# Optimization experiments

Hardware: AMD Instinct MI355X
Metric: run time of the kernel (lower is better)

Reference implementation:

```python
import jax, jax.numpy as jnp
import numpy as np

B, S, D, H = 4, 2048, 768, 12
HD = D // H  # head dim = 64


def setup_inputs() -> dict:
    key = jax.random.key(0)
    ks = jax.random.split(key, 8)
    w_scale = 0.02
    return {
        "x": jax.random.normal(ks[0], (B, S, D), dtype=jnp.float32),
        "Wq": jax.random.normal(ks[1], (D, D), dtype=jnp.float32) * w_scale,
        "bq": jnp.zeros((D,), dtype=jnp.float32),
        "Wk": jax.random.normal(ks[2], (D, D), dtype=jnp.float32) * w_scale,
        "Wv": jax.random.normal(ks[3], (D, D), dtype=jnp.float32) * w_scale,
        "bv": jnp.zeros((D,), dtype=jnp.float32),
        "Wo": jax.random.normal(ks[4], (D, D), dtype=jnp.float32) * w_scale,
        "bo": jnp.zeros((D,), dtype=jnp.float32),
    }


def reference(x, Wq, bq, Wk, Wv, bv, Wo, bo):
    # Self-attention branch (xa=None, no kv_cache), causal mask enabled.
    q = x @ Wq + bq                       # [B,S,D]; key proj has no bias
    k = x @ Wk
    v = x @ Wv + bv

    def split_heads(t):
        return t.reshape(B, S, H, HD).transpose(0, 2, 1, 3)  # [B,H,S,HD]

    q, k, v = split_heads(q), split_heads(k), split_heads(v)

    scale = float(HD) ** -0.5  # applied once to qk == (hd**-0.25 on q and k)
    qk = jnp.einsum("bhqd,bhkd->bhqk", q, k) * scale  # [B,H,S,S]

    # dynamic causal mask: -inf where kv index > q index
    causal = jnp.where(
        jnp.arange(S)[:, None] < jnp.arange(S)[None, :], -jnp.inf, 0.0
    ).astype(jnp.float32)
    qk = qk + causal

    w = jax.nn.softmax(qk.astype(jnp.float32), axis=-1).astype(q.dtype)
    out = jnp.einsum("bhqk,bhkd->bhqd", w, v)          # [B,H,S,HD]
    out = out.transpose(0, 2, 1, 3).reshape(B, S, D)    # [B,S,D]
    output = out @ Wo + bo
    return output, jax.lax.stop_gradient(qk)
```

## Files before the change

### kernel.cpp

```cpp
#include <hip/hip_runtime.h>
#include <cmath>

#define BB 4
#define SS 2048
#define DD 768
#define HH 12
#define HDD 64
#define MROWS (BB * SS)
#define NHEADS (BB * HH)

#define MASK_SENTINEL (-3.0e38f)

typedef float f32x4v __attribute__((ext_vector_type(4)));

__device__ __forceinline__ void nt_store4(float* p, float a, float b, float c,
                                          float d) {
    f32x4v t = {a, b, c, d};
    __builtin_nontemporal_store(t, reinterpret_cast<f32x4v*>(p));
}

template <bool SPLIT_HEADS>
__global__ __launch_bounds__(128) void gemm768(const float* __restrict__ A,
                                               const float* __restrict__ W,
                                               const float* __restrict__ bias,
                                               float* __restrict__ out) {
    __shared__ float As[16][132];
    __shared__ float Bs[16][68];

    const int tid = threadIdx.x;
    const int tx = tid & 7;
    const int ty = tid >> 3;
    const int m0 = blockIdx.y * 128;
    const int n0 = blockIdx.x * 64;

    const int br = tid >> 3;
    const int bc = (tid & 7) * 8;

    float acc[8][8] = {};

    for (int k0 = 0; k0 < 768; k0 += 16) {
        float4 av[4];
        const float* ap = &A[(size_t)(m0 + tid) * 768 + k0];
#pragma unroll
        for (int c = 0; c < 4; ++c) av[c] = reinterpret_cast<const float4*>(ap)[c];
        float4 bv[2];
        const float* bp = &W[(size_t)(k0 + br) * 768 + n0 + bc];
        bv[0] = reinterpret_cast<const float4*>(bp)[0];
        bv[1] = reinterpret_cast<const float4*>(bp)[1];

        if (k0 != 0) __syncthreads();
#pragma unroll
        for (int c = 0; c < 4; ++c) {
            As[c * 4 + 0][tid] = av[c].x;
            As[c * 4 + 1][tid] = av[c].y;
            As[c * 4 + 2][tid] = av[c].z;
            As[c * 4 + 3][tid] = av[c].w;
        }
        *reinterpret_cast<float4*>(&Bs[br][bc]) = bv[0];
        *reinterpret_cast<float4*>(&Bs[br][bc + 4]) = bv[1];
        __syncthreads();

#pragma unroll
        for (int kk = 0; kk < 16; ++kk) {
            const float4 a0 = *reinterpret_cast<const float4*>(&As[kk][ty * 8]);
            const float4 a1 = *reinterpret_cast<const float4*>(&As[kk][ty * 8 + 4]);
            const float4 b0 = *reinterpret_cast<const float4*>(&Bs[kk][tx * 8]);
            const float4 b1 = *reinterpret_cast<const float4*>(&Bs[kk][tx * 8 + 4]);
            const float af[8] = {a0.x, a0.y, a0.z, a0.w, a1.x, a1.y, a1.z, a1.w};
            const float bf[8] = {b0.x, b0.y, b0.z, b0.w, b1.x, b1.y, b1.z, b1.w};
#pragma unroll
            for (int i = 0; i < 8; ++i)
#pragma unroll
                for (int j = 0; j < 8; ++j)
                    acc[i][j] = fmaf(af[i], bf[j], acc[i][j]);
        }
    }

    float bn[8];
#pragma unroll
    for (int j = 0; j < 8; ++j) bn[j] = (bias != nullptr) ? bias[n0 + tx * 8 + j] : 0.f;

    const int h = n0 >> 6;
#pragma unroll
    for (int i = 0; i < 8; ++i) {
        const int m = m0 + ty * 8 + i;
        float r[8];
#pragma unroll
        for (int j = 0; j < 8; ++j) r[j] = acc[i][j] + bn[j];
        if (SPLIT_HEADS) {
            const int b = m >> 11;
            const int s = m & 2047;
            float* op = &out[(((size_t)(b * HH + h)) * SS + s) * HDD + tx * 8];
            *reinterpret_cast<float4*>(op) = make_float4(r[0], r[1], r[2], r[3]);
            *reinterpret_cast<float4*>(op + 4) = make_float4(r[4], r[5], r[6], r[7]);
        } else {
            float* op = &out[(size_t)m * 768 + n0 + tx * 8];
            *reinterpret_cast<float4*>(op) = make_float4(r[0], r[1], r[2], r[3]);
            *reinterpret_cast<float4*>(op + 4) = make_float4(r[4], r[5], r[6], r[7]);
        }
    }
}

__global__ __launch_bounds__(256) void attn_flash(const float* __restrict__ q,
                                                  const float* __restrict__ k,
                                                  const float* __restrict__ v,
                                                  float* __restrict__ qk_out,
                                                  float* __restrict__ attn_out) {
    __shared__ float Ks[64][68];
    __shared__ float Vs[64][68];

    const int tid = threadIdx.x;
    const int oct = tid & 7;
    const int rg = (tid >> 3) & 31;
    const int d0 = oct * 8;
    const int pair = blockIdx.x;
    const int bh = blockIdx.y;
    const size_t head_base = (size_t)bh * SS * HDD;
    const float scale = 0.125f;
    const int b_idx = bh / HH;
    const int h_idx = bh % HH;

    const int sr = tid >> 2;
    const int scb = (tid & 3) * 16;

    const int rsel = oct >> 2;
    const int g = oct & 3;

#pragma unroll 1
    for (int leg = 0; leg < 2; ++leg) {
        const int tq = (leg == 0) ? (31 - pair) : pair;
        const int q0 = tq * 64;
        const int qr0 = q0 + rg;
        const int qr1 = q0 + rg + 32;

        float4 q0reg[2], q1reg[2];
        {
            const float* qp0 = q + head_base + (size_t)qr0 * HDD + d0;
            const float* qp1 = q + head_base + (size_t)qr1 * HDD + d0;
            q0reg[0] = reinterpret_cast<const float4*>(qp0)[0];
            q0reg[1] = reinterpret_cast<const float4*>(qp0)[1];
            q1reg[0] = reinterpret_cast<const float4*>(qp1)[0];
            q1reg[1] = reinterpret_cast<const float4*>(qp1)[1];
        }

        float4 o0[2], o1[2];
#pragma unroll
        for (int c = 0; c < 2; ++c) {
            o0[c] = make_float4(0.f, 0.f, 0.f, 0.f);
            o1[c] = make_float4(0.f, 0.f, 0.f, 0.f);
        }
        float m0i = -INFINITY, l0 = 0.f;
        float m1i = -INFINITY, l1 = 0.f;

        float* qk_row0 = qk_out + ((size_t)bh * SS + qr0) * SS;
        float* qk_row1 = qk_out + ((size_t)bh * SS + qr1) * SS;

        const int kt_end = tq + 1;

        for (int kt = 0; kt < kt_end; ++kt) {
            float4 kreg[4], vreg[4];
            {
                const float* kp = k + head_base + (size_t)(kt * 64 + sr) * HDD + scb;
                const float* vp = v + head_base + (size_t)(kt * 64 + sr) * HDD + scb;
#pragma unroll
                for (int i = 0; i < 4; ++i) {
                    kreg[i] = reinterpret_cast<const float4*>(kp)[i];
                    vreg[i] = reinterpret_cast<const float4*>(vp)[i];
                }
            }
            __syncthreads();
#pragma unroll
            for (int i = 0; i < 4; ++i) {
                *reinterpret_cast<float4*>(&Ks[sr][scb + i * 4]) = kreg[i];
                *reinterpret_cast<float4*>(&Vs[sr][scb + i * 4]) = vreg[i];
            }
            __syncthreads();

            for (int jc = 0; jc < 64; jc += 16) {
                float s0[16], s1[16];
#pragma unroll
                for (int jj = 0; jj < 16; ++jj) {
                    const int j = jc + jj;
                    const float4 kv0 = *reinterpret_cast<const float4*>(&Ks[j][d0]);
                    const float4 kv1 =
                        *reinterpret_cast<const float4*>(&Ks[j][d0 + 4]);
                    float a0 = 0.f, a1 = 0.f;
                    a0 = fmaf(q0reg[0].x, kv0.x, a0);
                    a0 = fmaf(q0reg[0].y, kv0.y, a0);
                    a0 = fmaf(q0reg[0].z, kv0.z, a0);
                    a0 = fmaf(q0reg[0].w, kv0.w, a0);
                    a0 = fmaf(q0reg[1].x, kv1.x, a0);
                    a0 = fmaf(q0reg[1].y, kv1.y, a0);
                    a0 = fmaf(q0reg[1].z, kv1.z, a0);
                    a0 = fmaf(q0reg[1].w, kv1.w, a0);
                    a1 = fmaf(q1reg[0].x, kv0.x, a1);
                    a1 = fmaf(q1reg[0].y, kv0.y, a1);
                    a1 = fmaf(q1reg[0].z, kv0.z, a1);
                    a1 = fmaf(q1reg[0].w, kv0.w, a1);
                    a1 = fmaf(q1reg[1].x, kv1.x, a1);
                    a1 = fmaf(q1reg[1].y, kv1.y, a1);
                    a1 = fmaf(q1reg[1].z, kv1.z, a1);
                    a1 = fmaf(q1reg[1].w, kv1.w, a1);
                    a0 += __shfl_xor(a0, 1);
                    a0 += __shfl_xor(a0, 2);
                    a0 += __shfl_xor(a0, 4);
                    a1 += __shfl_xor(a1, 1);
                    a1 += __shfl_xor(a1, 2);
                    a1 += __shfl_xor(a1, 4);
                    const int jg = kt * 64 + j;
                    s0[jj] = (jg > qr0) ? -INFINITY : a0 * scale;
                    s1[jj] = (jg > qr1) ? -INFINITY : a1 * scale;
                }

                {
                    float w[4];
#pragma unroll
                    for (int t = 0; t < 4; ++t) {
                        const float x01 = (g & 1) ? s0[4 + t] : s0[t];
                        const float x23 = (g & 1) ? s0[12 + t] : s0[8 + t];
                        const float xs = (g & 2) ? x23 : x01;
                        const float y01 = (g & 1) ? s1[4 + t] : s1[t];
                        const float y23 = (g & 1) ? s1[12 + t] : s1[8 + t];
                        const float ys = (g & 2) ? y23 : y01;
                        w[t] = fmaxf(rsel ? ys : xs, MASK_SENTINEL);
                    }
                    float* dst = (rsel ? qk_row1 : qk_row0) + kt * 64 + jc + g * 4;
                    nt_store4(dst, w[0], w[1], w[2], w[3]);
                }

                float mc0 = s0[0], mc1 = s1[0];
#pragma unroll
                for (int jj = 1; jj < 16; ++jj) {
                    mc0 = fmaxf(mc0, s0[jj]);
                    mc1 = fmaxf(mc1, s1[jj]);
                }
                const float mn0 = fmaxf(m0i, mc0);
                const float mn1 = fmaxf(m1i, mc1);
                const bool dead0 = (mn0 == -INFINITY);
                const bool dead1 = (mn1 == -INFINITY);
                const float alpha0 = dead0 ? 1.f : __expf(m0i - mn0);
                const float alpha1 = dead1 ? 1.f : __expf(m1i - mn1);
                const float sub0 = dead0 ? 0.f : mn0;
                const float sub1 = dead1 ? 0.f : mn1;
                m0i = mn0;
                m1i = mn1;
                float ps0 = 0.f, ps1 = 0.f;
#pragma unroll
                for (int jj = 0; jj < 16; ++jj) {
                    s0[jj] = __expf(s0[jj] - sub0);
                    s1[jj] = __expf(s1[jj] - sub1);
                    ps0 += s0[jj];
                    ps1 += s1[jj];
                }
                l0 = l0 * alpha0 + ps0;
                l1 = l1 * alpha1 + ps1;
#pragma unroll
                for (int c = 0; c < 2; ++c) {
                    o0[c].x *= alpha0; o0[c].y *= alpha0;
                    o0[c].z *= alpha0; o0[c].w *= alpha0;
                    o1[c].x *= alpha1; o1[c].y *= alpha1;
                    o1[c].z *= alpha1; o1[c].w *= alpha1;
                }
#pragma unroll
                for (int jj = 0; jj < 16; ++jj) {
                    const float4 vv0 =
                        *reinterpret_cast<const float4*>(&Vs[jc + jj][d0]);
                    const float4 vv1 =
                        *reinterpret_cast<const float4*>(&Vs[jc + jj][d0 + 4]);
                    const float p0 = s0[jj];
                    const float p1 = s1[jj];
                    o0[0].x = fmaf(p0, vv0.x, o0[0].x);
                    o0[0].y = fmaf(p0, vv0.y, o0[0].y);
                    o0[0].z = fmaf(p0, vv0.z, o0[0].z);
                    o0[0].w = fmaf(p0, vv0.w, o0[0].w);
                    o0[1].x = fmaf(p0, vv1.x, o0[1].x);
                    o0[1].y = fmaf(p0, vv1.y, o0[1].y);
                    o0[1].z = fmaf(p0, vv1.z, o0[1].z);
                    o0[1].w = fmaf(p0, vv1.w, o0[1].w);
                    o1[0].x = fmaf(p1, vv0.x, o1[0].x);
                    o1[0].y = fmaf(p1, vv0.y, o1[0].y);
                    o1[0].z = fmaf(p1, vv0.z, o1[0].z);
                    o1[0].w = fmaf(p1, vv0.w, o1[0].w);
                    o1[1].x = fmaf(p1, vv1.x, o1[1].x);
                    o1[1].y = fmaf(p1, vv1.y, o1[1].y);
                    o1[1].z = fmaf(p1, vv1.z, o1[1].z);
                    o1[1].w = fmaf(p1, vv1.w, o1[1].w);
                }
            }
        }

        for (int base = kt_end * 64; base < SS; base += 32) {
            nt_store4(&qk_row0[base + oct * 4], MASK_SENTINEL, MASK_SENTINEL,
                      MASK_SENTINEL, MASK_SENTINEL);
            nt_store4(&qk_row1[base + oct * 4], MASK_SENTINEL, MASK_SENTINEL,
                      MASK_SENTINEL, MASK_SENTINEL);
        }

        const float inv0 = 1.0f / l0;
        const float inv1 = 1.0f / l1;
        float* op0 = attn_out + ((size_t)(b_idx * SS + qr0)) * DD + h_idx * HDD + d0;
        float* op1 = attn_out + ((size_t)(b_idx * SS + qr1)) * DD + h_idx * HDD + d0;
#pragma unroll
        for (int c = 0; c < 2; ++c) {
            float4 t0 = o0[c], t1 = o1[c];
            t0.x *= inv0; t0.y *= inv0; t0.z *= inv0; t0.w *= inv0;
            t1.x *= inv1; t1.y *= inv1; t1.z *= inv1; t1.w *= inv1;
            reinterpret_cast<float4*>(op0)[c] = t0;
            reinterpret_cast<float4*>(op1)[c] = t1;
        }
    }
}

extern "C" void kernel_launch(void* const* d_in, const int* in_sizes, int n_in,
                              void* d_out, int out_size, void* d_ws, size_t ws_size,
                              hipStream_t stream) {
    const float* x = (const float*)d_in[0];
    const float* Wq = (const float*)d_in[1];
    const float* bq = (const float*)d_in[2];
    const float* Wk = (const float*)d_in[3];
    const float* Wv = (const float*)d_in[4];
    const float* bv = (const float*)d_in[5];
    const float* Wo = (const float*)d_in[6];
    const float* bo = (const float*)d_in[7];

    float* out = (float*)d_out;
    float* qk = out + (size_t)BB * SS * DD;

    const size_t seg = (size_t)BB * SS * DD;
    float* qws = (float*)d_ws;
    float* kws = qws + seg;
    float* vws = qws + 2 * seg;
    float* aws = qws + 3 * seg;

    const dim3 gblk(128);
    const dim3 ggrid(DD / 64, MROWS / 128);

    gemm768<true><<<ggrid, gblk, 0, stream>>>(x, Wq, bq, qws);
    gemm768<true><<<ggrid, gblk, 0, stream>>>(x, Wk, nullptr, kws);
    gemm768<true><<<ggrid, gblk, 0, stream>>>(x, Wv, bv, vws);

    attn_flash<<<dim3(16, NHEADS), dim3(256), 0, stream>>>(qws, kws, vws, qk, aws);

    gemm768<false><<<ggrid, gblk, 0, stream>>>(aws, Wo, bo, out);
}
```

Before: 2.772 ms.

## Convert projections to fp16 MFMA GEMMs with pre-converted transposed weights

Replaces the fp32 SIMT projection GEMMs with an fp16 MFMA 16x16x32 kernel. Activations and weights are first converted to fp16, with the weights also transposed, in separate kernels. The attention kernel now writes its output in fp16 so the output projection can consume it directly. It also drops the nontemporal stores on the qk matrix in favour of plain float4 stores. Precision drops to fp16 inputs, and the GEMM epilogue now uses scalar, less coalesced stores.

```diff
diff --git a/kernel.cpp b/kernel.cpp
--- a/kernel.cpp
+++ b/kernel.cpp
@@ -11,92 +11,141 @@
 
 #define MASK_SENTINEL (-3.0e38f)
 
-typedef float f32x4v __attribute__((ext_vector_type(4)));
-
-__device__ __forceinline__ void nt_store4(float* p, float a, float b, float c,
-                                          float d) {
-    f32x4v t = {a, b, c, d};
-    __builtin_nontemporal_store(t, reinterpret_cast<f32x4v*>(p));
+typedef _Float16 f16;
+typedef _Float16 f16x8 __attribute__((ext_vector_type(8)));
+typedef float f32x4 __attribute__((ext_vector_type(4)));
+
+__global__ __launch_bounds__(256) void cvt_f32_f16(const float* __restrict__ in,
+                                                   f16* __restrict__ out, int n8) {
+    const int i = blockIdx.x * 256 + threadIdx.x;
+    if (i >= n8) return;
+    const float4 v0 = reinterpret_cast<const float4*>(in)[i * 2];
+    const float4 v1 = reinterpret_cast<const float4*>(in)[i * 2 + 1];
+    const f16x8 r = {(f16)v0.x, (f16)v0.y, (f16)v0.z, (f16)v0.w,
+                     (f16)v1.x, (f16)v1.y, (f16)v1.z, (f16)v1.w};
+    reinterpret_cast<f16x8*>(out)[i] = r;
 }
 
+__global__ __launch_bounds__(256) void cvt_w_t(const float* __restrict__ w0,
+                                               const float* __restrict__ w1,
+                                               const float* __restrict__ w2,
+                                               const float* __restrict__ w3,
+                                               f16* __restrict__ o0,
+                                               f16* __restrict__ o1,
+                                               f16* __restrict__ o2,
+                                               f16* __restrict__ o3) {
+    const float* W;
+    f16* O;
+    switch (blockIdx.z) {
+        case 0: W = w0; O = o0; break;
+        case 1: W = w1; O = o1; break;
+        case 2: W = w2; O = o2; break;
+        default: W = w3; O = o3; break;
+    }
+    const int k0 = blockIdx.y * 64;
+    const int n0 = blockIdx.x * 64;
+    const int kr = threadIdx.x >> 4;
+    const int nc = (threadIdx.x & 15) * 4;
+#pragma unroll
+    for (int stepk = 0; stepk < 64; stepk += 16) {
+        const int kk = k0 + kr + stepk;
+        const float4 v =
+            *reinterpret_cast<const float4*>(&W[(size_t)kk * 768 + n0 + nc]);
+        O[(size_t)(n0 + nc + 0) * 768 + kk] = (f16)v.x;
+        O[(size_t)(n0 + nc + 1) * 768 + kk] = (f16)v.y;
+        O[(size_t)(n0 + nc + 2) * 768 + kk] = (f16)v.z;
+        O[(size_t)(n0 + nc + 3) * 768 + kk] = (f16)v.w;
+    }
+}
+
 template <bool SPLIT_HEADS>
-__global__ __launch_bounds__(128) void gemm768(const float* __restrict__ A,
-                                               const float* __restrict__ W,
-                                               const float* __restrict__ bias,
-                                               float* __restrict__ out) {
-    __shared__ float As[16][132];
-    __shared__ float Bs[16][68];
+__global__ __launch_bounds__(256) void gemm_mfma(const f16* __restrict__ A,
+                                                 const f16* __restrict__ Bt,
+                                                 const float* __restrict__ bias,
+                                                 float* __restrict__ out) {
+    __shared__ __align__(16) f16 As[128][72];
+    __shared__ __align__(16) f16 Bs[64][72];
 
     const int tid = threadIdx.x;
-    const int tx = tid & 7;
-    const int ty = tid >> 3;
     const int m0 = blockIdx.y * 128;
     const int n0 = blockIdx.x * 64;
-
-    const int br = tid >> 3;
-    const int bc = (tid & 7) * 8;
-
-    float acc[8][8] = {};
-
-    for (int k0 = 0; k0 < 768; k0 += 16) {
-        float4 av[4];
-        const float* ap = &A[(size_t)(m0 + tid) * 768 + k0];
-#pragma unroll
-        for (int c = 0; c < 4; ++c) av[c] = reinterpret_cast<const float4*>(ap)[c];
-        float4 bv[2];
-        const float* bp = &W[(size_t)(k0 + br) * 768 + n0 + bc];
-        bv[0] = reinterpret_cast<const float4*>(bp)[0];
-        bv[1] = reinterpret_cast<const float4*>(bp)[1];
-
-        if (k0 != 0) __syncthreads();
-#pragma unroll
-        for (int c = 0; c < 4; ++c) {
-            As[c * 4 + 0][tid] = av[c].x;
-            As[c * 4 + 1][tid] = av[c].y;
-            As[c * 4 + 2][tid] = av[c].z;
-            As[c * 4 + 3][tid] = av[c].w;
-        }
-        *reinterpret_cast<float4*>(&Bs[br][bc]) = bv[0];
-        *reinterpret_cast<float4*>(&Bs[br][bc + 4]) = bv[1];
+    const int wave = tid >> 6;
+    const int lane = tid & 63;
+    const int wm = wave >> 1;
+    const int wn = wave & 1;
+    const int lr = lane & 15;
+    const int lg = lane >> 4;
+
+    const int ar = tid >> 1;
+    const int ac = (tid & 1) * 32;
+    const int br = tid >> 2;
+    const int bc = (tid & 3) * 16;
+
+    f32x4 acc[4][2];
+#pragma unroll
+    for (int m = 0; m < 4; ++m)
+#pragma unroll
+        for (int n = 0; n < 2; ++n) acc[m][n] = (f32x4){0.f, 0.f, 0.f, 0.f};
+
+    for (int kt = 0; kt < 12; ++kt) {
+        const int k0 = kt * 64;
+        uint4 ag[4], bg[2];
+        {
+            const f16* ap = A + (size_t)(m0 + ar) * 768 + k0 + ac;
+#pragma unroll
+            for (int i = 0; i < 4; ++i) ag[i] = reinterpret_cast<const uint4*>(ap)[i];
+            const f16* bp = Bt + (size_t)(n0 + br) * 768 + k0 + bc;
+            bg[0] = reinterpret_cast<const uint4*>(bp)[0];
+            bg[1] = reinterpret_cast<const uint4*>(bp)[1];
+        }
         __syncthreads();
-
-#pragma unroll
-        for (int kk = 0; kk < 16; ++kk) {
-            const float4 a0 = *reinterpret_cast<const float4*>(&As[kk][ty * 8]);
-            const float4 a1 = *reinterpret_cast<const float4*>(&As[kk][ty * 8 + 4]);
-            const float4 b0 = *reinterpret_cast<const float4*>(&Bs[kk][tx * 8]);
-            const float4 b1 = *reinterpret_cast<const float4*>(&Bs[kk][tx * 8 + 4]);
-            const float af[8] = {a0.x, a0.y, a0.z, a0.w, a1.x, a1.y, a1.z, a1.w};
-            const float bf[8] = {b0.x, b0.y, b0.z, b0.w, b1.x, b1.y, b1.z, b1.w};
-#pragma unroll
-            for (int i = 0; i < 8; ++i)
-#pragma unroll
-                for (int j = 0; j < 8; ++j)
-                    acc[i][j] = fmaf(af[i], bf[j], acc[i][j]);
+#pragma unroll
+        for (int i = 0; i < 4; ++i)
+            *reinterpret_cast<uint4*>(&As[ar][ac + i * 8]) = ag[i];
+        *reinterpret_cast<uint4*>(&Bs[br][bc]) = bg[0];
+        *reinterpret_cast<uint4*>(&Bs[br][bc + 8]) = bg[1];
+        __syncthreads();
+
+#pragma unroll
+        for (int s = 0; s < 2; ++s) {
+            f16x8 af[4], bf[2];
+#pragma unroll
+            for (int m = 0; m < 4; ++m)
+                af[m] = *reinterpret_cast<const f16x8*>(
+                    &As[wm * 64 + m * 16 + lr][s * 32 + lg * 8]);
+#pragma unroll
+            for (int n = 0; n < 2; ++n)
+                bf[n] = *reinterpret_cast<const f16x8*>(
+                    &Bs[wn * 32 + n * 16 + lr][s * 32 + lg * 8]);
+#pragma unroll
+            for (int m = 0; m < 4; ++m)
+#pragma unroll
+                for (int n = 0; n < 2; ++n)
+                    acc[m][n] = __builtin_amdgcn_mfma_f32_16x16x32_f16(
+                        af[m], bf[n], acc[m][n], 0, 0, 0);
         }
     }
 
-    float bn[8];
-#pragma unroll
-    for (int j = 0; j < 8; ++j) bn[j] = (bias != nullptr) ? bias[n0 + tx * 8 + j] : 0.f;
-
     const int h = n0 >> 6;
 #pragma unroll
-    for (int i = 0; i < 8; ++i) {
-        const int m = m0 + ty * 8 + i;
-        float r[8];
-#pragma unroll
-        for (int j = 0; j < 8; ++j) r[j] = acc[i][j] + bn[j];
-        if (SPLIT_HEADS) {
-            const int b = m >> 11;
-            const int s = m & 2047;
-            float* op = &out[(((size_t)(b * HH + h)) * SS + s) * HDD + tx * 8];
-            *reinterpret_cast<float4*>(op) = make_float4(r[0], r[1], r[2], r[3]);
-            *reinterpret_cast<float4*>(op + 4) = make_float4(r[4], r[5], r[6], r[7]);
-        } else {
-            float* op = &out[(size_t)m * 768 + n0 + tx * 8];
-            *reinterpret_cast<float4*>(op) = make_float4(r[0], r[1], r[2], r[3]);
-            *reinterpret_cast<float4*>(op + 4) = make_float4(r[4], r[5], r[6], r[7]);
+    for (int m = 0; m < 4; ++m) {
+#pragma unroll
+        for (int n = 0; n < 2; ++n) {
+            const int col = n0 + wn * 32 + n * 16 + lr;
+            const float bv = (bias != nullptr) ? bias[col] : 0.f;
+#pragma unroll
+            for (int j = 0; j < 4; ++j) {
+                const int row = m0 + wm * 64 + m * 16 + lg * 4 + j;
+                const float val = acc[m][n][j] + bv;
+                if (SPLIT_HEADS) {
+                    const int b = row >> 11;
+                    const int s = row & 2047;
+                    const int hd = col & 63;
+                    out[(((size_t)(b * HH + h)) * SS + s) * HDD + hd] = val;
+                } else {
+                    out[(size_t)row * 768 + col] = val;
+                }
+            }
         }
     }
 }
@@ -105,7 +154,7 @@
                                                   const float* __restrict__ k,
                                                   const float* __restrict__ v,
                                                   float* __restrict__ qk_out,
-                                                  float* __restrict__ attn_out) {
+                                                  f16* __restrict__ attn_out) {
     __shared__ float Ks[64][68];
     __shared__ float Vs[64][68];
 
@@ -225,7 +274,8 @@
                         w[t] = fmaxf(rsel ? ys : xs, MASK_SENTINEL);
                     }
                     float* dst = (rsel ? qk_row1 : qk_row0) + kt * 64 + jc + g * 4;
-                    nt_store4(dst, w[0], w[1], w[2], w[3]);
+                    *reinterpret_cast<float4*>(dst) =
+                        make_float4(w[0], w[1], w[2], w[3]);
                 }
 
                 float mc0 = s0[0], mc1 = s1[0];
@@ -289,25 +339,27 @@
             }
         }
 
+        const float4 sent4 = make_float4(MASK_SENTINEL, MASK_SENTINEL,
+                                         MASK_SENTINEL, MASK_SENTINEL);
         for (int base = kt_end * 64; base < SS; base += 32) {
-            nt_store4(&qk_row0[base + oct * 4], MASK_SENTINEL, MASK_SENTINEL,
-                      MASK_SENTINEL, MASK_SENTINEL);
-            nt_store4(&qk_row1[base + oct * 4], MASK_SENTINEL, MASK_SENTINEL,
-                      MASK_SENTINEL, MASK_SENTINEL);
+            *reinterpret_cast<float4*>(&qk_row0[base + oct * 4]) = sent4;
+            *reinterpret_cast<float4*>(&qk_row1[base + oct * 4]) = sent4;
         }
 
         const float inv0 = 1.0f / l0;
         const float inv1 = 1.0f / l1;
-        float* op0 = attn_out + ((size_t)(b_idx * SS + qr0)) * DD + h_idx * HDD + d0;
-        float* op1 = attn_out + ((size_t)(b_idx * SS + qr1)) * DD + h_idx * HDD + d0;
-#pragma unroll
-        for (int c = 0; c < 2; ++c) {
-            float4 t0 = o0[c], t1 = o1[c];
-            t0.x *= inv0; t0.y *= inv0; t0.z *= inv0; t0.w *= inv0;
-            t1.x *= inv1; t1.y *= inv1; t1.z *= inv1; t1.w *= inv1;
-            reinterpret_cast<float4*>(op0)[c] = t0;
-            reinterpret_cast<float4*>(op1)[c] = t1;
-        }
+        f16* op0 = attn_out + ((size_t)(b_idx * SS + qr0)) * DD + h_idx * HDD + d0;
+        f16* op1 = attn_out + ((size_t)(b_idx * SS + qr1)) * DD + h_idx * HDD + d0;
+        const f16x8 r0 = {(f16)(o0[0].x * inv0), (f16)(o0[0].y * inv0),
+                          (f16)(o0[0].z * inv0), (f16)(o0[0].w * inv0),
+                          (f16)(o0[1].x * inv0), (f16)(o0[1].y * inv0),
+                          (f16)(o0[1].z * inv0), (f16)(o0[1].w * inv0)};
+        const f16x8 r1 = {(f16)(o1[0].x * inv1), (f16)(o1[0].y * inv1),
+                          (f16)(o1[0].z * inv1), (f16)(o1[0].w * inv1),
+                          (f16)(o1[1].x * inv1), (f16)(o1[1].y * inv1),
+                          (f16)(o1[1].z * inv1), (f16)(o1[1].w * inv1)};
+        *reinterpret_cast<f16x8*>(op0) = r0;
+        *reinterpret_cast<f16x8*>(op1) = r1;
     }
 }
 
@@ -330,16 +382,26 @@
     float* qws = (float*)d_ws;
     float* kws = qws + seg;
     float* vws = qws + 2 * seg;
-    float* aws = qws + 3 * seg;
-
-    const dim3 gblk(128);
+    f16* xh = (f16*)(qws + 3 * seg);
+    f16* ah = xh;
+    f16* wtq = xh + seg;
+    f16* wtk = wtq + 768 * 768;
+    f16* wtv = wtk + 768 * 768;
+    f16* wto = wtv + 768 * 768;
+
+    cvt_f32_f16<<<dim3((int)(seg / 8 / 256)), dim3(256), 0, stream>>>(x, xh,
+                                                                      (int)(seg / 8));
+    cvt_w_t<<<dim3(12, 12, 4), dim3(256), 0, stream>>>(Wq, Wk, Wv, Wo, wtq, wtk,
+                                                       wtv, wto);
+
+    const dim3 gblk(256);
     const dim3 ggrid(DD / 64, MROWS / 128);
 
-    gemm768<true><<<ggrid, gblk, 0, stream>>>(x, Wq, bq, qws);
-    gemm768<true><<<ggrid, gblk, 0, stream>>>(x, Wk, nullptr, kws);
-    gemm768<true><<<ggrid, gblk, 0, stream>>>(x, Wv, bv, vws);
-
-    attn_flash<<<dim3(16, NHEADS), dim3(256), 0, stream>>>(qws, kws, vws, qk, aws);
-
-    gemm768<false><<<ggrid, gblk, 0, stream>>>(aws, Wo, bo, out);
+    gemm_mfma<true><<<ggrid, gblk, 0, stream>>>(xh, wtq, bq, qws);
+    gemm_mfma<true><<<ggrid, gblk, 0, stream>>>(xh, wtk, nullptr, kws);
+    gemm_mfma<true><<<ggrid, gblk, 0, stream>>>(xh, wtv, bv, vws);
+
+    attn_flash<<<dim3(16, NHEADS), dim3(256), 0, stream>>>(qws, kws, vws, qk, ah);
+
+    gemm_mfma<false><<<ggrid, gblk, 0, stream>>>(ah, wto, bo, out);
 }
```

Result: no change. 2.794 ms (+0.8%).
